# Kernel optimization log

Measured on AMD Instinct MI355X. Metric: run time of the kernel, lower is better.

## Reference

```python
import jax, jax.numpy as jnp
import numpy as np

# ---- fixed sizes ----
N_IN = 100_000          # total inner nodes
NODES_PER_INNER = 50    # nodes per inner graph
N_OUT = N_IN // NODES_PER_INNER          # 2000 outer nodes (= num inner graphs)
NODES_PER_OUTER = 125   # outer nodes per outer graph
B = N_OUT // NODES_PER_OUTER             # 16 graphs in the batch
DEG = 8
E_IN = N_IN * DEG        # 800_000 inner edges
E_OUT = N_OUT * DEG      # 16_000 outer edges
IN_FEATS = 64
OUT_FEATS = 64
H = 128                  # h_feats = [128]*6
NUM_CLASSES = 10


def _rand_edges(key, n_graphs, nodes_per_graph, edges_per_graph):
    """Random edges that stay inside each graph of a batched graph."""
    k1, k2 = jax.random.split(key)
    src_l = jax.random.randint(k1, (n_graphs, edges_per_graph), 0, nodes_per_graph)
    dst_l = jax.random.randint(k2, (n_graphs, edges_per_graph), 0, nodes_per_graph)
    off = (jnp.arange(n_graphs) * nodes_per_graph)[:, None]
    return ((src_l + off).reshape(-1).astype(jnp.int32),
            (dst_l + off).reshape(-1).astype(jnp.int32))


def setup_inputs() -> dict:
    key = jax.random.key(0)
    ks = jax.random.split(key, 24)
    inner_src, inner_dst = _rand_edges(ks[0], N_OUT, NODES_PER_INNER, E_IN // N_OUT)
    outer_src, outer_dst = _rand_edges(ks[1], B, NODES_PER_OUTER, E_OUT // B)

    def w(k, fan_in, fan_out):
        return jax.random.normal(k, (fan_in, fan_out), jnp.float32) * (1.0 / np.sqrt(fan_in))

    inp = {
        "in_layer_feat": jax.random.normal(ks[2], (N_IN, IN_FEATS), jnp.float32),
        "out_layer_feat": jax.random.normal(ks[3], (N_OUT, OUT_FEATS), jnp.float32),
        "inner_ew": jax.random.uniform(ks[4], (E_IN,), jnp.float32) + 0.5,
        "outer_ew": jax.random.uniform(ks[5], (E_OUT,), jnp.float32) + 0.5,
        "W1": w(ks[6], IN_FEATS, H),        "b1": jnp.zeros((H,), jnp.float32),
        "W2": w(ks[7], H, H),               "b2": jnp.zeros((H,), jnp.float32),
        "W3": w(ks[8], OUT_FEATS + H, H),   "b3": jnp.zeros((H,), jnp.float32),
        "W4": w(ks[9], H, H),               "b4": jnp.zeros((H,), jnp.float32),
        "W5": w(ks[10], H, H),              "b5": jnp.zeros((H,), jnp.float32),
        "W6": w(ks[11], H, H),              "b6": jnp.zeros((H,), jnp.float32),
        "Wc": w(ks[12], H, NUM_CLASSES),    "bc": jnp.zeros((NUM_CLASSES,), jnp.float32),
        "inner_src": inner_src, "inner_dst": inner_dst,
        "outer_src": outer_src, "outer_dst": outer_dst,
        "inner_node_graph": (jnp.arange(N_IN) // NODES_PER_INNER).astype(jnp.int32),
        "outer_node_graph": (jnp.arange(N_OUT) // NODES_PER_OUTER).astype(jnp.int32),
    }
    return inp


def graph_conv(src, dst, ew, x, W, b, n_nodes):
    """DGL GraphConv, norm='both', weighted aggregation, zero-in-degree allowed."""
    ones = jnp.ones(src.shape[0], x.dtype)
    deg_out = jnp.clip(jax.ops.segment_sum(ones, src, num_segments=n_nodes), 1.0)
    deg_in = jnp.clip(jax.ops.segment_sum(ones, dst, num_segments=n_nodes), 1.0)
    xs = x * jax.lax.rsqrt(deg_out)[:, None]                      # src normalization
    msg = xs[src] * ew[:, None]                                   # u_mul_e
    agg = jax.ops.segment_sum(msg, dst, num_segments=n_nodes)     # copy_e -> sum
    agg = agg * jax.lax.rsqrt(deg_in)[:, None]                    # dst normalization
    return agg @ W + b


def mean_nodes(h, node_graph, n_graphs, nodes_per_graph):
    return jax.ops.segment_sum(h, node_graph, num_segments=n_graphs) / nodes_per_graph


def reference(in_layer_feat, out_layer_feat, inner_ew, outer_ew,
              W1, b1, W2, b2, W3, b3, W4, b4, W5, b5, W6, b6, Wc, bc,
              inner_src, inner_dst, outer_src, outer_dst,
              inner_node_graph, outer_node_graph):
    # inner-graph message passing
    h = jax.nn.relu(graph_conv(inner_src, inner_dst, inner_ew, in_layer_feat, W1, b1, N_IN))
    h = jax.nn.relu(graph_conv(inner_src, inner_dst, inner_ew, h, W2, b2, N_IN))
    reduced = mean_nodes(h, inner_node_graph, N_OUT, float(NODES_PER_INNER))  # [N_OUT, H]
    merged = jnp.concatenate([out_layer_feat, reduced], axis=-1)              # [N_OUT, OUT_FEATS+H]
    # outer-graph message passing
    h = jax.nn.relu(graph_conv(outer_src, outer_dst, outer_ew, merged, W3, b3, N_OUT))
    h = jax.nn.relu(graph_conv(outer_src, outer_dst, outer_ew, h, W4, b4, N_OUT))
    h = jax.nn.relu(graph_conv(outer_src, outer_dst, outer_ew, h, W5, b5, N_OUT))
    h = jax.nn.relu(graph_conv(outer_src, outer_dst, outer_ew, h, W6, b6, N_OUT))
    hg = mean_nodes(h, outer_node_graph, B, float(NODES_PER_OUTER))           # [B, H]
    return hg @ Wc + bc                                                       # [B, NUM_CLASSES]
```

## Files before the change

### kernel.cpp

```cpp
#include <hip/hip_runtime.h>

#define NPI 50
#define EPI 400
#define NPO 125
#define EPO 1000
#define N_IN 100000
#define N_OUT 2000
#define NB 16
#define NC 10

typedef _Float16 half_t;
typedef _Float16 f16x8 __attribute__((ext_vector_type(8)));
typedef float f32x4 __attribute__((ext_vector_type(4)));

#define MFMA(a, b, c) __builtin_amdgcn_mfma_f32_16x16x32_f16(a, b, c, 0, 0, 0)

__device__ __forceinline__ f16x8 lds_ld8(const half_t* base, int row, int k, int strideB) {
    return *(const f16x8*)((const char*)base + row * strideB + ((k * 2) ^ ((row & 7) << 4)));
}
__device__ __forceinline__ void lds_st1(half_t* base, int row, int col, int strideB, float v) {
    *(half_t*)((char*)base + row * strideB + ((col * 2) ^ ((row & 7) << 4))) = (half_t)v;
}
__device__ __forceinline__ void lds_st1h(half_t* base, int row, int col, int strideB, half_t v) {
    *(half_t*)((char*)base + row * strideB + ((col * 2) ^ ((row & 7) << 4))) = v;
}
__device__ __forceinline__ void lds_st8(half_t* base, int row, int k, int strideB, f16x8 v) {
    *(f16x8*)((char*)base + row * strideB + ((k * 2) ^ ((row & 7) << 4))) = v;
}
__device__ __forceinline__ f16x8 scr_ld8(const half_t* base, int row, int k) {
    return *(const f16x8*)((const char*)base + row * 64 + ((k * 2) ^ ((row & 3) << 4)));
}
__device__ __forceinline__ void scr_st1(half_t* base, int row, int col, float v) {
    *(half_t*)((char*)base + row * 64 + ((col * 2) ^ ((row & 3) << 4))) = (half_t)v;
}

__global__ __launch_bounds__(256) void k_pre(
    const float* __restrict__ W1, const float* __restrict__ W2,
    const float* __restrict__ W3, const float* __restrict__ W4,
    const float* __restrict__ W5, const float* __restrict__ W6,
    half_t* __restrict__ WT1, half_t* __restrict__ WT2,
    half_t* __restrict__ WT3, half_t* __restrict__ WT4,
    half_t* __restrict__ WT5, half_t* __restrict__ WT6,
    const float* __restrict__ ew, const int* __restrict__ esrc,
    const int* __restrict__ edst, half_t* __restrict__ Aout)
{
    __shared__ float Af[NPO * NPO];
    __shared__ int cO[NPO], cI[NPO];
    __shared__ float rso[NPO], rsi[NPO];
    const int t = threadIdx.x;

    if (blockIdx.x < 384) {
        int i = blockIdx.x * 256 + t;
        const float* src; half_t* dst; int K;
        if      (i < 8192)  { src = W1; dst = WT1; K = 64; }
        else if (i < 24576) { src = W2; dst = WT2; K = 128; i -= 8192; }
        else if (i < 49152) { src = W3; dst = WT3; K = 192; i -= 24576; }
        else if (i < 65536) { src = W4; dst = WT4; K = 128; i -= 49152; }
        else if (i < 81920) { src = W5; dst = WT5; K = 128; i -= 65536; }
        else                { src = W6; dst = WT6; K = 128; i -= 81920; }
        int c = i & 127, k = i >> 7;
        dst[c * K + k] = (half_t)src[k * 128 + c];
        return;
    }

    const int g = blockIdx.x - 384;
    const int nb = g * NPO, eb = g * EPO;
    for (int i = t; i < NPO * NPO; i += 256) Af[i] = 0.f;
    if (t < NPO) { cO[t] = 0; cI[t] = 0; }
    __syncthreads();
    for (int e = t; e < EPO; e += 256) {
        int s = esrc[eb + e] - nb, d = edst[eb + e] - nb;
        atomicAdd(&Af[d * NPO + s], ew[eb + e]);
        atomicAdd(&cO[s], 1); atomicAdd(&cI[d], 1);
    }
    __syncthreads();
    if (t < NPO) {
        rso[t] = rsqrtf((float)max(cO[t], 1));
        rsi[t] = rsqrtf((float)max(cI[t], 1));
    }
    __syncthreads();
    for (int i = t; i < 128 * 16; i += 256) {
        int d = i >> 4, s0 = (i & 15) * 8;
        f16x8 v;
        #pragma unroll
        for (int j = 0; j < 8; j++) {
            int s = s0 + j;
            float x = (d < NPO && s < NPO) ? Af[d * NPO + s] * rsi[d] * rso[s] : 0.f;
            v[j] = (half_t)x;
        }
        *(f16x8*)&Aout[(size_t)g * 16384 + d * 128 + s0] = v;
    }
}

__global__ __launch_bounds__(256, 5) void k_inner(
    const float* __restrict__ X, const float* __restrict__ outfeat,
    const float* __restrict__ ew, const int* __restrict__ esrc,
    const int* __restrict__ edst,
    const half_t* __restrict__ WT1, const float* __restrict__ b1,
    const half_t* __restrict__ WT2, const float* __restrict__ b2,
    half_t* __restrict__ merged)
{
    __shared__ alignas(16) char smem[29696];
    half_t* Ah  = (half_t*)smem;
    half_t* R2  = (half_t*)(smem + 8192);
    float*  Af  = (float*)(smem + 8192);
    half_t* scr = (half_t*)(smem + 24576);
    float*  pool= (float*)(smem + 28672);
    int*    cO  = (int*)(smem + 29184);
    int*    cI  = (int*)(smem + 29440);

    const int g = blockIdx.x, t = threadIdx.x;
    const int w = t >> 6, l = t & 63, lr = l & 15, lk = l >> 4;
    const int nb = g * NPI, eb = g * EPI;
    half_t* scrw = scr + w * 512;

    float ofv = (t < 64) ? outfeat[(size_t)g * 64 + t] : 0.f;
    int s0e, d0e; float w0e;
    { int e = eb + t; s0e = esrc[e] - nb; d0e = edst[e] - nb; w0e = ew[e]; }
    int s1e = 0, d1e = 0; float w1e = 0.f;
    const bool e1v = (t + 256 < EPI);
    if (e1v) { int e = eb + t + 256; s1e = esrc[e] - nb; d1e = edst[e] - nb; w1e = ew[e]; }

    if (t < 64) { cO[t] = 0; cI[t] = 0; }
    if (t >= 64 && t < 192) pool[t - 64] = 0.f;
    for (int i = t; i < 4096; i += 256) Af[i] = 0.f;
    __syncthreads();

    atomicAdd(&Af[d0e * 64 + s0e], w0e);
    atomicAdd(&cO[s0e], 1); atomicAdd(&cI[d0e], 1);
    if (e1v) {
        atomicAdd(&Af[d1e * 64 + s1e], w1e);
        atomicAdd(&cO[s1e], 1); atomicAdd(&cI[d1e], 1);
    }
    __syncthreads();

    const int srow = t >> 2, qc = t & 3;
    float4 xr0 = {0,0,0,0}, xr1 = xr0, xr2 = xr0, xr3 = xr0;
    if (srow < NPI) {
        const float* xp = &X[(size_t)(nb + srow) * 64 + qc * 16];
        xr0 = *(const float4*)(xp + 0);
        xr1 = *(const float4*)(xp + 4);
        xr2 = *(const float4*)(xp + 8);
        xr3 = *(const float4*)(xp + 12);
    }

    for (int i = t; i < 4096; i += 256) {
        int d = i >> 6, s = i & 63;
        float v = Af[i] * rsqrtf((float)max(cI[d], 1)) * rsqrtf((float)max(cO[s], 1));
        lds_st1(Ah, d, s, 128, v);
    }
    __syncthreads();

    {
        float xv[16] = {xr0.x,xr0.y,xr0.z,xr0.w, xr1.x,xr1.y,xr1.z,xr1.w,
                        xr2.x,xr2.y,xr2.z,xr2.w, xr3.x,xr3.y,xr3.z,xr3.w};
        #pragma unroll
        for (int i = 0; i < 16; i++) lds_st1(R2, qc * 16 + i, srow, 128, xv[i]);
    }
    __syncthreads();

    f32x4 hacc[8] = {};
    #pragma unroll
    for (int kf = 0; kf < 2; kf++) {
        #pragma unroll
        for (int j = 0; j < 2; j++) {
            const int ft = kf * 2 + j;
            f32x4 tacc = {};
            #pragma unroll
            for (int ks = 0; ks < 2; ks++) {
                f16x8 a = lds_ld8(Ah, w * 16 + lr, ks * 32 + lk * 8, 128);
                f16x8 b = lds_ld8(R2, ft * 16 + lr, ks * 32 + lk * 8, 128);
                tacc = MFMA(a, b, tacc);
            }
            #pragma unroll
            for (int q = 0; q < 4; q++) scr_st1(scrw, lk * 4 + q, j * 16 + lr, tacc[q]);
        }
        f16x8 a1 = scr_ld8(scrw, lr, lk * 8);
        #pragma unroll
        for (int nt = 0; nt < 8; nt++) {
            f16x8 b = *(const f16x8*)&WT1[(nt * 16 + lr) * 64 + kf * 32 + lk * 8];
            hacc[nt] = MFMA(a1, b, hacc[nt]);
        }
    }
    __syncthreads();
    #pragma unroll
    for (int nt = 0; nt < 8; nt++) {
        int c = nt * 16 + lr;
        float bb = b1[c];
        #pragma unroll
        for (int q = 0; q < 4; q++)
            lds_st1(R2, c, w * 16 + lk * 4 + q, 128, fmaxf(hacc[nt][q] + bb, 0.f));
    }
    __syncthreads();

    f32x4 h2[8] = {};
    #pragma unroll
    for (int kf = 0; kf < 4; kf++) {
        #pragma unroll
        for (int j = 0; j < 2; j++) {
            const int ft = kf * 2 + j;
            f32x4 tacc = {};
            #pragma unroll
            for (int ks = 0; ks < 2; ks++) {
                f16x8 a = lds_ld8(Ah, w * 16 + lr, ks * 32 + lk * 8, 128);
                f16x8 b = lds_ld8(R2, ft * 16 + lr, ks * 32 + lk * 8, 128);
                tacc = MFMA(a, b, tacc);
            }
            #pragma unroll
            for (int q = 0; q < 4; q++) scr_st1(scrw, lk * 4 + q, j * 16 + lr, tacc[q]);
        }
        f16x8 a1 = scr_ld8(scrw, lr, lk * 8);
        #pragma unroll
        for (int nt = 0; nt < 8; nt++) {
            f16x8 b = *(const f16x8*)&WT2[(nt * 16 + lr) * 128 + kf * 32 + lk * 8];
            h2[nt] = MFMA(a1, b, h2[nt]);
        }
    }
    #pragma unroll
    for (int nt = 0; nt < 8; nt++) {
        int c = nt * 16 + lr;
        float bb = b2[c];
        float ps = 0.f;
        #pragma unroll
        for (int q = 0; q < 4; q++) {
            int m = w * 16 + lk * 4 + q;
            float v = fmaxf(h2[nt][q] + bb, 0.f);
            ps += (m < NPI) ? v : 0.f;
        }
        ps += __shfl_xor(ps, 16);
        ps += __shfl_xor(ps, 32);
        if (lk == 0) atomicAdd(&pool[c], ps);
    }
    __syncthreads();
    if (t < 64) merged[(size_t)g * 192 + t] = (half_t)ofv;
    else if (t < 192) merged[(size_t)g * 192 + t] = (half_t)(pool[t - 64] * (1.f / NPI));
}

template <int FIN, bool STAGE, bool LAST>
__device__ __forceinline__ void outer_layer(
    const half_t* AgL, const half_t* __restrict__ mg,
    const half_t* __restrict__ WT, const float* __restrict__ bias,
    half_t* bufP, half_t* bufQ, float* pool,
    int w, int lr, int lk, int t)
{
    f32x4 hacc[8] = {};
    constexpr int NCH = FIN / 64;
    #pragma unroll
    for (int ch = 0; ch < NCH; ch++) {
        if constexpr (STAGE) {
            __syncthreads();
            for (int i = t; i < 1024; i += 512) {
                int s = i >> 3, fo = (i & 7) * 8;
                f16x8 hv = {};
                if (s < NPO) hv = *(const f16x8*)&mg[(size_t)s * 192 + ch * 64 + fo];
                #pragma unroll
                for (int j = 0; j < 8; j++) lds_st1h(bufP, fo + j, s, 256, hv[j]);
            }
            __syncthreads();
        }
        const int rb = STAGE ? 0 : ch * 64;
        f32x4 tacc[4] = {};
        #pragma unroll
        for (int ks = 0; ks < 4; ks++) {
            f16x8 a = lds_ld8(AgL, w * 16 + lr, ks * 32 + lk * 8, 256);
            #pragma unroll
            for (int nt = 0; nt < 4; nt++) {
                f16x8 b = lds_ld8(bufP, rb + nt * 16 + lr, ks * 32 + lk * 8, 256);
                tacc[nt] = MFMA(a, b, tacc[nt]);
            }
        }
        #pragma unroll
        for (int nt = 0; nt < 4; nt++)
            #pragma unroll
            for (int q = 0; q < 4; q++)
                lds_st1(bufQ, w * 16 + lk * 4 + q, nt * 16 + lr, 128, tacc[nt][q]);
        #pragma unroll
        for (int ks2 = 0; ks2 < 2; ks2++) {
            f16x8 a1 = lds_ld8(bufQ, w * 16 + lr, ks2 * 32 + lk * 8, 128);
            #pragma unroll
            for (int nt = 0; nt < 8; nt++) {
                f16x8 b = *(const f16x8*)&WT[(nt * 16 + lr) * FIN + ch * 64 + ks2 * 32 + lk * 8];
                hacc[nt] = MFMA(a1, b, hacc[nt]);
            }
        }
    }
    __syncthreads();
    if constexpr (!LAST) {
        #pragma unroll
        for (int nt = 0; nt < 8; nt++) {
            int c = nt * 16 + lr;
            float bb = bias[c];
            #pragma unroll
            for (int q = 0; q < 4; q++)
                lds_st1(bufP, c, w * 16 + lk * 4 + q, 256, fmaxf(hacc[nt][q] + bb, 0.f));
        }
        __syncthreads();
    } else {
        #pragma unroll
        for (int nt = 0; nt < 8; nt++) {
            int c = nt * 16 + lr;
            float bb = bias[c];
            float ps = 0.f;
            #pragma unroll
            for (int q = 0; q < 4; q++) {
                int d = w * 16 + lk * 4 + q;
                float v = fmaxf(hacc[nt][q] + bb, 0.f);
                ps += (d < NPO) ? v : 0.f;
            }
            ps += __shfl_xor(ps, 16);
            ps += __shfl_xor(ps, 32);
            if (lk == 0) atomicAdd(&pool[c], ps);
        }
        __syncthreads();
    }
}

__global__ __launch_bounds__(512) void k_outer(
    const half_t* __restrict__ Aout, const half_t* __restrict__ merged,
    const half_t* __restrict__ WT3, const float* __restrict__ b3,
    const half_t* __restrict__ WT4, const float* __restrict__ b4,
    const half_t* __restrict__ WT5, const float* __restrict__ b5,
    const half_t* __restrict__ WT6, const float* __restrict__ b6,
    const float* __restrict__ Wc, const float* __restrict__ bc,
    float* __restrict__ out)
{
    __shared__ alignas(16) char smem[82432];
    half_t* AgL  = (half_t*)smem;
    half_t* bufP = (half_t*)(smem + 32768);
    half_t* bufQ = (half_t*)(smem + 65536);
    float*  pool = (float*)(smem + 81920);

    const int g = blockIdx.x, t = threadIdx.x;
    const int w = t >> 6, l = t & 63, lr = l & 15, lk = l >> 4;
    const half_t* mg = merged + (size_t)g * NPO * 192;

    for (int i = t; i < 2048; i += 512) {
        int row = i >> 4, k0 = (i & 15) * 8;
        f16x8 v = *(const f16x8*)&Aout[(size_t)g * 16384 + row * 128 + k0];
        lds_st8(AgL, row, k0, 256, v);
    }
    if (t < 128) pool[t] = 0.f;
    __syncthreads();

    outer_layer<192, true,  false>(AgL, mg, WT3, b3, bufP, bufQ, pool, w, lr, lk, t);
    outer_layer<128, false, false>(AgL, nullptr, WT4, b4, bufP, bufQ, pool, w, lr, lk, t);
    outer_layer<128, false, false>(AgL, nullptr, WT5, b5, bufP, bufQ, pool, w, lr, lk, t);
    outer_layer<128, false, true >(AgL, nullptr, WT6, b6, bufP, bufQ, pool, w, lr, lk, t);

    if (t < NC) {
        float acc = bc[t];
        for (int k = 0; k < 128; k++)
            acc = fmaf(pool[k] * (1.f / NPO), Wc[k * NC + t], acc);
        out[g * NC + t] = acc;
    }
}

extern "C" void kernel_launch(void* const* d_in, const int* in_sizes, int n_in,
                              void* d_out, int out_size, void* d_ws, size_t ws_size,
                              hipStream_t stream)
{
    const float* X       = (const float*)d_in[0];
    const float* outfeat = (const float*)d_in[1];
    const float* iew     = (const float*)d_in[2];
    const float* oew     = (const float*)d_in[3];
    const float* W1 = (const float*)d_in[4];  const float* b1 = (const float*)d_in[5];
    const float* W2 = (const float*)d_in[6];  const float* b2 = (const float*)d_in[7];
    const float* W3 = (const float*)d_in[8];  const float* b3 = (const float*)d_in[9];
    const float* W4 = (const float*)d_in[10]; const float* b4 = (const float*)d_in[11];
    const float* W5 = (const float*)d_in[12]; const float* b5 = (const float*)d_in[13];
    const float* W6 = (const float*)d_in[14]; const float* b6 = (const float*)d_in[15];
    const float* Wc = (const float*)d_in[16]; const float* bc = (const float*)d_in[17];
    const int* isrc = (const int*)d_in[18];   const int* idst = (const int*)d_in[19];
    const int* osrc = (const int*)d_in[20];   const int* odst = (const int*)d_in[21];

    char* base = (char*)d_ws;
    half_t* WT1 = (half_t*)(base + 0);
    half_t* WT2 = (half_t*)(base + 16384);
    half_t* WT3 = (half_t*)(base + 49152);
    half_t* WT4 = (half_t*)(base + 98304);
    half_t* WT5 = (half_t*)(base + 131072);
    half_t* WT6 = (half_t*)(base + 163840);
    half_t* AoutG  = (half_t*)(base + 196608);
    half_t* merged = (half_t*)(base + 720896);

    k_pre<<<400, 256, 0, stream>>>(W1, W2, W3, W4, W5, W6,
                                   WT1, WT2, WT3, WT4, WT5, WT6,
                                   oew, osrc, odst, AoutG);
    k_inner<<<N_OUT, 256, 0, stream>>>(X, outfeat, iew, isrc, idst,
                                       WT1, b1, WT2, b2, merged);
    k_outer<<<NB, 512, 0, stream>>>(AoutG, merged, WT3, b3, WT4, b4,
                                    WT5, b5, WT6, b6, Wc, bc, (float*)d_out);
}
```

Before: 125.8 us.

## Split fused inner-graph kernel into adjacency, transform GEMM, and aggregation kernels

```diff
diff --git a/kernel.cpp b/kernel.cpp
--- a/kernel.cpp
+++ b/kernel.cpp
@@ -26,12 +26,6 @@
 }
 __device__ __forceinline__ void lds_st8(half_t* base, int row, int k, int strideB, f16x8 v) {
     *(f16x8*)((char*)base + row * strideB + ((k * 2) ^ ((row & 7) << 4))) = v;
-}
-__device__ __forceinline__ f16x8 scr_ld8(const half_t* base, int row, int k) {
-    return *(const f16x8*)((const char*)base + row * 64 + ((k * 2) ^ ((row & 3) << 4)));
-}
-__device__ __forceinline__ void scr_st1(half_t* base, int row, int col, float v) {
-    *(half_t*)((char*)base + row * 64 + ((col * 2) ^ ((row & 3) << 4))) = (half_t)v;
 }
 
 __global__ __launch_bounds__(256) void k_pre(
@@ -92,29 +86,15 @@
     }
 }
 
-__global__ __launch_bounds__(256, 5) void k_inner(
-    const float* __restrict__ X, const float* __restrict__ outfeat,
+__global__ __launch_bounds__(256) void k_adjI(
     const float* __restrict__ ew, const int* __restrict__ esrc,
-    const int* __restrict__ edst,
-    const half_t* __restrict__ WT1, const float* __restrict__ b1,
-    const half_t* __restrict__ WT2, const float* __restrict__ b2,
-    half_t* __restrict__ merged)
-{
-    __shared__ alignas(16) char smem[29696];
-    half_t* Ah  = (half_t*)smem;
-    half_t* R2  = (half_t*)(smem + 8192);
-    float*  Af  = (float*)(smem + 8192);
-    half_t* scr = (half_t*)(smem + 24576);
-    float*  pool= (float*)(smem + 28672);
-    int*    cO  = (int*)(smem + 29184);
-    int*    cI  = (int*)(smem + 29440);
-
+    const int* __restrict__ edst, half_t* __restrict__ AinG)
+{
+    __shared__ float Af[64 * 64];
+    __shared__ int cO[64], cI[64];
     const int g = blockIdx.x, t = threadIdx.x;
-    const int w = t >> 6, l = t & 63, lr = l & 15, lk = l >> 4;
     const int nb = g * NPI, eb = g * EPI;
-    half_t* scrw = scr + w * 512;
-
-    float ofv = (t < 64) ? outfeat[(size_t)g * 64 + t] : 0.f;
+
     int s0e, d0e; float w0e;
     { int e = eb + t; s0e = esrc[e] - nb; d0e = edst[e] - nb; w0e = ew[e]; }
     int s1e = 0, d1e = 0; float w1e = 0.f;
@@ -122,10 +102,8 @@
     if (e1v) { int e = eb + t + 256; s1e = esrc[e] - nb; d1e = edst[e] - nb; w1e = ew[e]; }
 
     if (t < 64) { cO[t] = 0; cI[t] = 0; }
-    if (t >= 64 && t < 192) pool[t - 64] = 0.f;
     for (int i = t; i < 4096; i += 256) Af[i] = 0.f;
     __syncthreads();
-
     atomicAdd(&Af[d0e * 64 + s0e], w0e);
     atomicAdd(&cO[s0e], 1); atomicAdd(&cI[d0e], 1);
     if (e1v) {
@@ -133,107 +111,157 @@
         atomicAdd(&cO[s1e], 1); atomicAdd(&cI[d1e], 1);
     }
     __syncthreads();
-
-    const int srow = t >> 2, qc = t & 3;
-    float4 xr0 = {0,0,0,0}, xr1 = xr0, xr2 = xr0, xr3 = xr0;
-    if (srow < NPI) {
-        const float* xp = &X[(size_t)(nb + srow) * 64 + qc * 16];
-        xr0 = *(const float4*)(xp + 0);
-        xr1 = *(const float4*)(xp + 4);
-        xr2 = *(const float4*)(xp + 8);
-        xr3 = *(const float4*)(xp + 12);
-    }
-
-    for (int i = t; i < 4096; i += 256) {
-        int d = i >> 6, s = i & 63;
-        float v = Af[i] * rsqrtf((float)max(cI[d], 1)) * rsqrtf((float)max(cO[s], 1));
-        lds_st1(Ah, d, s, 128, v);
-    }
-    __syncthreads();
-
-    {
-        float xv[16] = {xr0.x,xr0.y,xr0.z,xr0.w, xr1.x,xr1.y,xr1.z,xr1.w,
-                        xr2.x,xr2.y,xr2.z,xr2.w, xr3.x,xr3.y,xr3.z,xr3.w};
-        #pragma unroll
-        for (int i = 0; i < 16; i++) lds_st1(R2, qc * 16 + i, srow, 128, xv[i]);
-    }
-    __syncthreads();
-
-    f32x4 hacc[8] = {};
-    #pragma unroll
-    for (int kf = 0; kf < 2; kf++) {
-        #pragma unroll
-        for (int j = 0; j < 2; j++) {
-            const int ft = kf * 2 + j;
-            f32x4 tacc = {};
-            #pragma unroll
-            for (int ks = 0; ks < 2; ks++) {
-                f16x8 a = lds_ld8(Ah, w * 16 + lr, ks * 32 + lk * 8, 128);
-                f16x8 b = lds_ld8(R2, ft * 16 + lr, ks * 32 + lk * 8, 128);
-                tacc = MFMA(a, b, tacc);
-            }
-            #pragma unroll
-            for (int q = 0; q < 4; q++) scr_st1(scrw, lk * 4 + q, j * 16 + lr, tacc[q]);
-        }
-        f16x8 a1 = scr_ld8(scrw, lr, lk * 8);
+    #pragma unroll
+    for (int j = 0; j < 2; j++) {
+        int id = t + j * 256;
+        int row = id >> 3, k0 = (id & 7) * 8;
+        float rsi_l = rsqrtf((float)max(cI[row], 1));
+        f16x8 v;
+        #pragma unroll
+        for (int jj = 0; jj < 8; jj++)
+            v[jj] = (half_t)(Af[row * 64 + k0 + jj] * rsi_l *
+                             rsqrtf((float)max(cO[k0 + jj], 1)));
+        *(f16x8*)&AinG[(size_t)g * 4096 + row * 64 + k0] = v;
+    }
+}
+
+template <int K, bool F32IN>
+__global__ __launch_bounds__(256) void k_gemmT(
+    const void* __restrict__ Ain, const half_t* __restrict__ BT,
+    half_t* __restrict__ YT)
+{
+    const int t = threadIdx.x, w = t >> 6, l = t & 63;
+    const int lr = l & 15, lk = l >> 4;
+    const int r0 = blockIdx.x * 128 + w * 32;
+
+    const int ra = r0 + lr, rb = r0 + 16 + lr;
+    const int xra = (ra >> 6) * 50 + min(ra & 63, 49);
+    const int xrb = (rb >> 6) * 50 + min(rb & 63, 49);
+
+    f32x4 acc[2][8] = {};
+    for (int ks = 0; ks < K / 32; ks++) {
+        const int ko = ks * 32 + lk * 8;
+        f16x8 a0, a1;
+        if constexpr (F32IN) {
+            const float* A = (const float*)Ain;
+            const float* pa = &A[(size_t)xra * K + ko];
+            const float* pb = &A[(size_t)xrb * K + ko];
+            #pragma unroll
+            for (int j = 0; j < 8; j++) { a0[j] = (half_t)pa[j]; a1[j] = (half_t)pb[j]; }
+        } else {
+            const half_t* A = (const half_t*)Ain;
+            a0 = *(const f16x8*)&A[(size_t)xra * K + ko];
+            a1 = *(const f16x8*)&A[(size_t)xrb * K + ko];
+        }
+        #pragma unroll
+        for (int ct = 0; ct < 8; ct++) {
+            f16x8 b = *(const f16x8*)&BT[(size_t)(ct * 16 + lr) * K + ko];
+            acc[0][ct] = MFMA(a0, b, acc[0][ct]);
+            acc[1][ct] = MFMA(a1, b, acc[1][ct]);
+        }
+    }
+    #pragma unroll
+    for (int rt = 0; rt < 2; rt++) {
+        #pragma unroll
+        for (int q = 0; q < 4; q++) {
+            int r = r0 + rt * 16 + lk * 4 + q;
+            int g = r >> 6, i = r & 63;
+            half_t* dst = &YT[(size_t)g * 8192 + i];
+            #pragma unroll
+            for (int ct = 0; ct < 8; ct++)
+                dst[(ct * 16 + lr) * 64] = (half_t)acc[rt][ct][q];
+        }
+    }
+}
+
+__global__ __launch_bounds__(256) void k_aggA(
+    const half_t* __restrict__ AinG, const half_t* __restrict__ Y1T,
+    const float* __restrict__ b1, half_t* __restrict__ h1)
+{
+    const int t = threadIdx.x, w = t >> 6, l = t & 63;
+    const int lr = l & 15, lk = l >> 4;
+    const int g = blockIdx.x * 4 + w;
+    const half_t* Ag = AinG + (size_t)g * 4096;
+    const half_t* Yg = Y1T + (size_t)g * 8192;
+
+    float bias[8];
+    #pragma unroll
+    for (int nt = 0; nt < 8; nt++) bias[nt] = b1[nt * 16 + lr];
+
+    #pragma unroll
+    for (int st = 0; st < 4; st++) {
+        f16x8 a0 = *(const f16x8*)&Ag[(st * 16 + lr) * 64 + lk * 8];
+        f16x8 a1 = *(const f16x8*)&Ag[(st * 16 + lr) * 64 + 32 + lk * 8];
+        f32x4 acc[8] = {};
         #pragma unroll
         for (int nt = 0; nt < 8; nt++) {
-            f16x8 b = *(const f16x8*)&WT1[(nt * 16 + lr) * 64 + kf * 32 + lk * 8];
-            hacc[nt] = MFMA(a1, b, hacc[nt]);
-        }
-    }
-    __syncthreads();
+            f16x8 b0 = *(const f16x8*)&Yg[(nt * 16 + lr) * 64 + lk * 8];
+            f16x8 b1f = *(const f16x8*)&Yg[(nt * 16 + lr) * 64 + 32 + lk * 8];
+            acc[nt] = MFMA(a0, b0, acc[nt]);
+            acc[nt] = MFMA(a1, b1f, acc[nt]);
+        }
+        #pragma unroll
+        for (int q = 0; q < 4; q++) {
+            int r = st * 16 + lk * 4 + q;
+            if (r < NPI) {
+                half_t* dst = &h1[((size_t)g * NPI + r) * 128];
+                #pragma unroll
+                for (int nt = 0; nt < 8; nt++)
+                    dst[nt * 16 + lr] = (half_t)fmaxf(acc[nt][q] + bias[nt], 0.f);
+            }
+        }
+    }
+}
+
+__global__ __launch_bounds__(256) void k_aggB(
+    const half_t* __restrict__ AinG, const half_t* __restrict__ Y2T,
+    const float* __restrict__ b2, const float* __restrict__ outfeat,
+    half_t* __restrict__ merged)
+{
+    const int t = threadIdx.x, w = t >> 6, l = t & 63;
+    const int lr = l & 15, lk = l >> 4;
+    const int g = blockIdx.x * 4 + w;
+    const half_t* Ag = AinG + (size_t)g * 4096;
+    const half_t* Yg = Y2T + (size_t)g * 8192;
+
+    float bias[8], psum[8];
+    #pragma unroll
+    for (int nt = 0; nt < 8; nt++) { bias[nt] = b2[nt * 16 + lr]; psum[nt] = 0.f; }
+
+    #pragma unroll
+    for (int st = 0; st < 4; st++) {
+        f16x8 a0 = *(const f16x8*)&Ag[(st * 16 + lr) * 64 + lk * 8];
+        f16x8 a1 = *(const f16x8*)&Ag[(st * 16 + lr) * 64 + 32 + lk * 8];
+        f32x4 acc[8] = {};
+        #pragma unroll
+        for (int nt = 0; nt < 8; nt++) {
+            f16x8 b0 = *(const f16x8*)&Yg[(nt * 16 + lr) * 64 + lk * 8];
+            f16x8 b1f = *(const f16x8*)&Yg[(nt * 16 + lr) * 64 + 32 + lk * 8];
+            acc[nt] = MFMA(a0, b0, acc[nt]);
+            acc[nt] = MFMA(a1, b1f, acc[nt]);
+        }
+        #pragma unroll
+        for (int nt = 0; nt < 8; nt++) {
+            #pragma unroll
+            for (int q = 0; q < 4; q++) {
+                int r = st * 16 + lk * 4 + q;
+                float v = fmaxf(acc[nt][q] + bias[nt], 0.f);
+                psum[nt] += (r < NPI) ? v : 0.f;
+            }
+        }
+    }
     #pragma unroll
     for (int nt = 0; nt < 8; nt++) {
-        int c = nt * 16 + lr;
-        float bb = b1[c];
-        #pragma unroll
-        for (int q = 0; q < 4; q++)
-            lds_st1(R2, c, w * 16 + lk * 4 + q, 128, fmaxf(hacc[nt][q] + bb, 0.f));
-    }
-    __syncthreads();
-
-    f32x4 h2[8] = {};
-    #pragma unroll
-    for (int kf = 0; kf < 4; kf++) {
-        #pragma unroll
-        for (int j = 0; j < 2; j++) {
-            const int ft = kf * 2 + j;
-            f32x4 tacc = {};
-            #pragma unroll
-            for (int ks = 0; ks < 2; ks++) {
-                f16x8 a = lds_ld8(Ah, w * 16 + lr, ks * 32 + lk * 8, 128);
-                f16x8 b = lds_ld8(R2, ft * 16 + lr, ks * 32 + lk * 8, 128);
-                tacc = MFMA(a, b, tacc);
-            }
-            #pragma unroll
-            for (int q = 0; q < 4; q++) scr_st1(scrw, lk * 4 + q, j * 16 + lr, tacc[q]);
-        }
-        f16x8 a1 = scr_ld8(scrw, lr, lk * 8);
-        #pragma unroll
-        for (int nt = 0; nt < 8; nt++) {
-            f16x8 b = *(const f16x8*)&WT2[(nt * 16 + lr) * 128 + kf * 32 + lk * 8];
-            h2[nt] = MFMA(a1, b, h2[nt]);
-        }
-    }
-    #pragma unroll
-    for (int nt = 0; nt < 8; nt++) {
-        int c = nt * 16 + lr;
-        float bb = b2[c];
-        float ps = 0.f;
-        #pragma unroll
-        for (int q = 0; q < 4; q++) {
-            int m = w * 16 + lk * 4 + q;
-            float v = fmaxf(h2[nt][q] + bb, 0.f);
-            ps += (m < NPI) ? v : 0.f;
-        }
-        ps += __shfl_xor(ps, 16);
-        ps += __shfl_xor(ps, 32);
-        if (lk == 0) atomicAdd(&pool[c], ps);
-    }
-    __syncthreads();
-    if (t < 64) merged[(size_t)g * 192 + t] = (half_t)ofv;
-    else if (t < 192) merged[(size_t)g * 192 + t] = (half_t)(pool[t - 64] * (1.f / NPI));
+        psum[nt] += __shfl_xor(psum[nt], 16);
+        psum[nt] += __shfl_xor(psum[nt], 32);
+    }
+    merged[(size_t)g * 192 + l] = (half_t)outfeat[(size_t)g * 64 + l];
+    if (l < 16) {
+        #pragma unroll
+        for (int nt = 0; nt < 8; nt++)
+            merged[(size_t)g * 192 + 64 + nt * 16 + l] =
+                (half_t)(psum[nt] * (1.f / NPI));
+    }
 }
 
 template <int FIN, bool STAGE, bool LAST>
@@ -382,12 +410,18 @@
     half_t* WT6 = (half_t*)(base + 163840);
     half_t* AoutG  = (half_t*)(base + 196608);
     half_t* merged = (half_t*)(base + 720896);
+    half_t* AinG   = (half_t*)(base + 1490944);
+    half_t* YT     = (half_t*)(base + 17874944);
+    half_t* h1     = (half_t*)(base + 50642944);
 
     k_pre<<<400, 256, 0, stream>>>(W1, W2, W3, W4, W5, W6,
                                    WT1, WT2, WT3, WT4, WT5, WT6,
                                    oew, osrc, odst, AoutG);
-    k_inner<<<N_OUT, 256, 0, stream>>>(X, outfeat, iew, isrc, idst,
-                                       WT1, b1, WT2, b2, merged);
+    k_adjI<<<N_OUT, 256, 0, stream>>>(iew, isrc, idst, AinG);
+    k_gemmT<64, true><<<1000, 256, 0, stream>>>((const void*)X, WT1, YT);
+    k_aggA<<<500, 256, 0, stream>>>(AinG, YT, b1, h1);
+    k_gemmT<128, false><<<1000, 256, 0, stream>>>((const void*)h1, WT2, YT);
+    k_aggB<<<500, 256, 0, stream>>>(AinG, YT, b2, outfeat, merged);
     k_outer<<<NB, 512, 0, stream>>>(AoutG, merged, WT3, b3, WT4, b4,
                                     WT5, b5, WT6, b6, Wc, bc, (float*)d_out);
 }
```

Measured after the change: 153.2 us. 1.22x slower.
